# Optimization experiments

Measured on AMD Instinct MI355X. Metric: run time of the kernel, lower is better.

Reference implementation:

```python
import jax, jax.numpy as jnp
import numpy as np

# --- config (matches init_kwargs) ---
C = 1e-12
FILTER_LENGTH = 512
INPUT_SIZE = 8192
NUM_LAYERS = 4
BATCH = 4096

MIN_NORM = 1e-15
PROJ_EPS = 4e-3  # hgcn PoincareBall eps for float32


def _proj(x, c):
    # clip points to stay inside the Poincare ball
    norm = jnp.maximum(jnp.linalg.norm(x, axis=-1, keepdims=True), MIN_NORM)
    maxnorm = (1.0 - PROJ_EPS) / jnp.sqrt(c)
    return jnp.where(norm > maxnorm, x / norm * maxnorm, x)


def _expmap0(u, c):
    # proj_tan0 is identity on the Poincare ball
    sqrt_c = jnp.sqrt(c)
    u_norm = jnp.maximum(jnp.linalg.norm(u, axis=-1, keepdims=True), MIN_NORM)
    return jnp.tanh(sqrt_c * u_norm) * u / (sqrt_c * u_norm)


def _mobius_add(x, y, c):
    x2 = jnp.sum(x * x, axis=-1, keepdims=True)
    y2 = jnp.sum(y * y, axis=-1, keepdims=True)
    xy = jnp.sum(x * y, axis=-1, keepdims=True)
    num = (1.0 + 2.0 * c * xy + c * y2) * x + (1.0 - c * x2) * y
    denom = 1.0 + 2.0 * c * xy + c * c * x2 * y2
    return num / jnp.maximum(denom, MIN_NORM)


def setup_inputs() -> dict:
    key = jax.random.key(0)
    ks = jax.random.split(key, 2 + NUM_LAYERS)
    inp = {
        "hk": jax.random.normal(ks[0], (BATCH, INPUT_SIZE), dtype=jnp.float32),
        # torch.rand -> uniform [0,1)
        "w": jax.random.uniform(ks[1], (NUM_LAYERS, FILTER_LENGTH), dtype=jnp.float32),
    }
    for i in range(NUM_LAYERS):
        inp[f"bk{i}"] = jax.random.uniform(
            ks[2 + i], (INPUT_SIZE + (i + 1) * FILTER_LENGTH,), dtype=jnp.float32
        )
    return inp


def reference(hk, w, bk0, bk1, bk2, bk3):
    bks = [bk0, bk1, bk2, bk3]
    # full 1D convolution, batched over rows: out[b, j] = sum_l w[j-l] * v[b, l]
    conv1 = jax.vmap(lambda v, wi: jnp.convolve(v, wi, mode="full"), in_axes=(0, None))
    out = hk
    for i in range(NUM_LAYERS):
        v = out[:, :INPUT_SIZE]          # expansive_conv reads only first INPUT_SIZE entries
        conv = conv1(v, w[i])            # [B, INPUT_SIZE + FILTER_LENGTH - 1]
        pad = i * FILTER_LENGTH + 1      # zero tail up to conv_length = INPUT_SIZE + (i+1)*FL
        conv = jnp.pad(conv, ((0, 0), (0, pad)))
        hyp = _proj(_expmap0(conv, C), C)
        out = jax.nn.relu(_mobius_add(hyp, bks[i][None, :], C))
    return out
```

## Files before the change

kernel.cpp:

```cpp
#include <hip/hip_runtime.h>
#include <hip/hip_bf16.h>
#include <math.h>

#define TB 256
#define NW 4
#define TPW 9
#define VOFFH 512
#define SVH 9760
#define UMAX 81

typedef __attribute__((ext_vector_type(8))) short bf16x8;
typedef __attribute__((ext_vector_type(4))) float f32x4;

__device__ __forceinline__ short f2b(float x) {
    union { __hip_bfloat16 h; short s; } u;
    u.h = __float2bfloat16(x);
    return u.s;
}

__global__ __launch_bounds__(256) void y2_kernel(
    const float* __restrict__ bk0, const float* __restrict__ bk1,
    const float* __restrict__ bk2, const float* __restrict__ bk3,
    float* __restrict__ ws)
{
    const float* bks[4] = {bk0, bk1, bk2, bk3};
    const int i = blockIdx.x;
    const int L = 8192 + (i + 1) * 512;
    const float* b = bks[i];
    float s = 0.f;
    for (int n = threadIdx.x; n < L; n += 256) { float x = b[n]; s += x * x; }
    #pragma unroll
    for (int off = 32; off; off >>= 1) s += __shfl_down(s, off, 64);
    __shared__ float sp[4];
    if ((threadIdx.x & 63) == 0) sp[threadIdx.x >> 6] = s;
    __syncthreads();
    if (threadIdx.x == 0) ws[i] = sp[0] + sp[1] + sp[2] + sp[3];
}

__global__ __launch_bounds__(64) void prep_kernel(const float* __restrict__ w,
                                                  short* __restrict__ wtab)
{
    const int id   = blockIdx.x;
    const int layer = id / 17, ks = id % 17;
    const int lane = threadIdx.x;
    const int r    = lane & 15;
    const int kb   = ks * 32 + (lane >> 4) * 8;
    const float* wl = w + layer * 512;
    bf16x8 bb;
    #pragma unroll
    for (int jj = 0; jj < 8; ++jj) {
        const int idx = 512 + r - (kb + jj);
        const float val = (idx >= 0 && idx < 512) ? wl[idx] : 0.f;
        bb[jj] = f2b(val);
    }
    *(bf16x8*)(wtab + ((size_t)id * 64 + lane) * 8) = bb;
}

__global__ __launch_bounds__(TB, 3) void hdcnn_kernel(
    const float* __restrict__ hk, const short* __restrict__ wtab,
    const float* __restrict__ bk0, const float* __restrict__ bk1,
    const float* __restrict__ bk2, const float* __restrict__ bk3,
    const float* __restrict__ y2w, float* __restrict__ out)
{
    __shared__ __align__(16) short svb[SVH];
    __shared__ float sred[NW * 2];

    const int tid  = threadIdx.x;
    const int row  = blockIdx.x;
    const int lane = tid & 63;
    const int wv   = tid >> 6;
    const int jn   = lane & 15;
    const int kq   = lane >> 4;
    const int t0   = wv * TPW;

    {
        int* svi = (int*)svb;
        for (int i = tid; i < SVH / 2; i += TB) svi[i] = 0;
    }
    __syncthreads();

    {
        const float4* hrow = (const float4*)(hk + (size_t)row * 8192);
        for (int j = tid; j < 1024; j += TB) {
            float4 x0 = hrow[2 * j];
            float4 x1 = hrow[2 * j + 1];
            bf16x8 p;
            p[0] = f2b(x0.x); p[1] = f2b(x0.y); p[2] = f2b(x0.z); p[3] = f2b(x0.w);
            p[4] = f2b(x1.x); p[5] = f2b(x1.y); p[6] = f2b(x1.z); p[7] = f2b(x1.w);
            *(bf16x8*)(svb + VOFFH + 8 * j) = p;
        }
    }

    const int vbase = t0 * 256 + 16 * jn + 8 * kq;

    for (int layer = 0; layer < 4; ++layer) {
        const float* __restrict__ bk = (layer == 0) ? bk0 : (layer == 1) ? bk1
                                     : (layer == 2) ? bk2 : bk3;

        const short* wt = wtab + (size_t)layer * 8704 + lane * 8;
        bf16x8 wf[17];
        #pragma unroll
        for (int ks = 0; ks < 17; ++ks) wf[ks] = *(const bf16x8*)(wt + ks * 512);

        __syncthreads();

        f32x4 acc[TPW];
        #pragma unroll
        for (int dt = 0; dt < TPW; ++dt) acc[dt] = (f32x4){0.f, 0.f, 0.f, 0.f};

        #pragma unroll
        for (int u = 0; u < UMAX; ++u) {
            bf16x8 vf = *(const bf16x8*)(svb + vbase + 32 * u);
            const int dtlo = (u > 16) ? ((u - 9) >> 3) : 0;
            const int dthi = ((u >> 3) < TPW - 1) ? (u >> 3) : (TPW - 1);
            #pragma unroll
            for (int dt = dtlo; dt <= dthi; ++dt)
                acc[dt] = __builtin_amdgcn_mfma_f32_16x16x32_bf16(
                    wf[u - 8 * dt], vf, acc[dt], 0, 0, 0);
        }

        float sum2 = 0.f, sxy = 0.f;
        #pragma unroll
        for (int dt = 0; dt < TPW; ++dt) {
            if (t0 + dt < 34) {
                const int nb = (t0 + dt) * 256 + 16 * jn + 4 * kq;
                float4 b4 = *(const float4*)(bk + nb);
                sum2 = fmaf(acc[dt][0], acc[dt][0], sum2);
                sum2 = fmaf(acc[dt][1], acc[dt][1], sum2);
                sum2 = fmaf(acc[dt][2], acc[dt][2], sum2);
                sum2 = fmaf(acc[dt][3], acc[dt][3], sum2);
                sxy  = fmaf(acc[dt][0], b4.x, sxy);
                sxy  = fmaf(acc[dt][1], b4.y, sxy);
                sxy  = fmaf(acc[dt][2], b4.z, sxy);
                sxy  = fmaf(acc[dt][3], b4.w, sxy);
            }
        }
        #pragma unroll
        for (int off = 32; off; off >>= 1) {
            sum2 += __shfl_down(sum2, off, 64);
            sxy  += __shfl_down(sxy,  off, 64);
        }
        if (lane == 0) { sred[wv * 2] = sum2; sred[wv * 2 + 1] = sxy; }
        __syncthreads();
        float un2 = 0.f, xys = 0.f;
        #pragma unroll
        for (int i = 0; i < NW; ++i) { un2 += sred[2 * i]; xys += sred[2 * i + 1]; }

        const float Cc  = 1e-12f;
        const float un  = sqrtf(un2);
        const float unc = fmaxf(un, 1e-15f);
        const float aa  = 1e-6f * unc;
        const float f   = tanhf(aa) / aa;
        const float hn  = f * un;
        const float hnc = fmaxf(hn, 1e-15f);
        const float maxn = (1.0f - 0.004f) * 1.0e6f;
        const float s   = (hnc > maxn) ? f * (maxn / hnc) : f;
        const float x2  = s * s * un2;
        const float xy  = s * xys;
        const float y2  = y2w[layer];
        const float t2c = 2.f * Cc * xy;
        const float A   = 1.f + t2c + Cc * y2;
        const float B   = 1.f - Cc * x2;
        float D = 1.f + t2c + Cc * Cc * x2 * y2;
        D = fmaxf(D, 1e-15f);
        const float alpha = A * s / D;
        const float beta  = B / D;

        if (layer < 3) {
            #pragma unroll
            for (int dt = 0; dt < TPW; ++dt) {
                if (t0 + dt < 32) {
                    const int nb = (t0 + dt) * 256 + 16 * jn + 4 * kq;
                    float4 b4 = *(const float4*)(bk + nb);
                    short4 o;
                    o.x = f2b(fmaxf(alpha * acc[dt][0] + beta * b4.x, 0.f));
                    o.y = f2b(fmaxf(alpha * acc[dt][1] + beta * b4.y, 0.f));
                    o.z = f2b(fmaxf(alpha * acc[dt][2] + beta * b4.z, 0.f));
                    o.w = f2b(fmaxf(alpha * acc[dt][3] + beta * b4.w, 0.f));
                    *(short4*)(svb + VOFFH + nb) = o;
                }
            }
        } else {
            float* orow = out + (size_t)row * 10240;
            #pragma unroll
            for (int dt = 0; dt < TPW; ++dt) {
                if (t0 + dt < 34) {
                    const int nb = (t0 + dt) * 256 + 16 * jn + 4 * kq;
                    float4 b4 = *(const float4*)(bk + nb);
                    float4 o;
                    o.x = fmaxf(alpha * acc[dt][0] + beta * b4.x, 0.f);
                    o.y = fmaxf(alpha * acc[dt][1] + beta * b4.y, 0.f);
                    o.z = fmaxf(alpha * acc[dt][2] + beta * b4.z, 0.f);
                    o.w = fmaxf(alpha * acc[dt][3] + beta * b4.w, 0.f);
                    *(float4*)(orow + nb) = o;
                }
            }
            for (int n = 8704 + 4 * tid; n < 10240; n += 4 * TB) {
                float4 b4 = *(const float4*)(bk + n);
                float4 o;
                o.x = fmaxf(beta * b4.x, 0.f);
                o.y = fmaxf(beta * b4.y, 0.f);
                o.z = fmaxf(beta * b4.z, 0.f);
                o.w = fmaxf(beta * b4.w, 0.f);
                *(float4*)(orow + n) = o;
            }
        }
    }
}

extern "C" void kernel_launch(void* const* d_in, const int* in_sizes, int n_in,
                              void* d_out, int out_size, void* d_ws, size_t ws_size,
                              hipStream_t stream) {
    const float* hk  = (const float*)d_in[0];
    const float* w   = (const float*)d_in[1];
    const float* bk0 = (const float*)d_in[2];
    const float* bk1 = (const float*)d_in[3];
    const float* bk2 = (const float*)d_in[4];
    const float* bk3 = (const float*)d_in[5];
    float* out = (float*)d_out;
    float* ws  = (float*)d_ws;
    short* wtab = (short*)(ws + 4);

    y2_kernel<<<4, 256, 0, stream>>>(bk0, bk1, bk2, bk3, ws);
    prep_kernel<<<68, 64, 0, stream>>>(w, wtab);
    hdcnn_kernel<<<4096, TB, 0, stream>>>(hk, wtab, bk0, bk1, bk2, bk3, ws, out);
}
```

Measured before the change: 229.7 us.

## Replace per-step LDS loads with DPP row-shift reconstruction and skip idle tail steps

```diff
diff --git a/kernel.cpp b/kernel.cpp
--- a/kernel.cpp
+++ b/kernel.cpp
@@ -1,6 +1,7 @@
 #include <hip/hip_runtime.h>
 #include <hip/hip_bf16.h>
 #include <math.h>
+#include <utility>
 
 #define TB 256
 #define NW 4
@@ -8,14 +9,65 @@
 #define VOFFH 512
 #define SVH 9760
 #define UMAX 81
+#define UCUT 65
 
 typedef __attribute__((ext_vector_type(8))) short bf16x8;
+typedef __attribute__((ext_vector_type(4))) int   i32x4;
 typedef __attribute__((ext_vector_type(4))) float f32x4;
 
 __device__ __forceinline__ short f2b(float x) {
     union { __hip_bfloat16 h; short s; } u;
     u.h = __float2bfloat16(x);
     return u.s;
+}
+
+__device__ __forceinline__ void unused_marker() {}
+template<int CTRL>
+__device__ __forceinline__ bf16x8 dpp4(bf16x8 v) {
+    i32x4 s = *(i32x4*)&v;
+    i32x4 d;
+    d[0] = __builtin_amdgcn_update_dpp(0, s[0], CTRL, 0xf, 0xf, false);
+    d[1] = __builtin_amdgcn_update_dpp(0, s[1], CTRL, 0xf, 0xf, false);
+    d[2] = __builtin_amdgcn_update_dpp(0, s[2], CTRL, 0xf, 0xf, false);
+    d[3] = __builtin_amdgcn_update_dpp(0, s[3], CTRL, 0xf, 0xf, false);
+    return *(bf16x8*)&d;
+}
+
+struct Scan { bf16x8 W0, W1, W2; };
+
+template<int U>
+__device__ __forceinline__ void scan_step(Scan& S, f32x4 (&acc)[TPW],
+                                          const bf16x8 (&wf)[17],
+                                          const short* svb, int vbase, int jn) {
+    constexpr int r = U & 7;
+    constexpr int k = U >> 3;
+    bf16x8& A = (k % 3 == 0) ? S.W0 : (k % 3 == 1) ? S.W1 : S.W2;
+    bf16x8& B = ((k + 1) % 3 == 0) ? S.W0 : ((k + 1) % 3 == 1) ? S.W1 : S.W2;
+    bf16x8& C = ((k + 2) % 3 == 0) ? S.W0 : ((k + 2) % 3 == 1) ? S.W1 : S.W2;
+    if constexpr (r == 0 && U + 16 <= 88) {
+        C = *(const bf16x8*)(svb + vbase + 32 * (U + 16));
+    }
+    bf16x8 vf;
+    if constexpr (r == 0) {
+        vf = A;
+    } else {
+        bf16x8 a = dpp4<0x100 + 2 * r>(A);
+        bf16x8 b = dpp4<0x110 + (16 - 2 * r)>(B);
+        vf = (jn + 2 * r < 16) ? a : b;
+    }
+    constexpr int dtlo = (U > 16) ? ((U - 9) >> 3) : 0;
+    constexpr int dthi = ((U >> 3) < TPW - 1) ? (U >> 3) : (TPW - 1);
+    #pragma unroll
+    for (int dt = dtlo; dt <= dthi; ++dt)
+        acc[dt] = __builtin_amdgcn_mfma_f32_16x16x32_bf16(
+            wf[U - 8 * dt], vf, acc[dt], 0, 0, 0);
+}
+
+template<int OFF, int... Is>
+__device__ __forceinline__ void run_steps(std::integer_sequence<int, Is...>,
+        Scan& S, f32x4 (&acc)[TPW], const bf16x8 (&wf)[17],
+        const short* svb, int vbase, int jn) {
+    (scan_step<OFF + Is>(S, acc, wf, svb, vbase, jn), ...);
 }
 
 __global__ __launch_bounds__(256) void y2_kernel(
@@ -108,15 +160,15 @@
         #pragma unroll
         for (int dt = 0; dt < TPW; ++dt) acc[dt] = (f32x4){0.f, 0.f, 0.f, 0.f};
 
-        #pragma unroll
-        for (int u = 0; u < UMAX; ++u) {
-            bf16x8 vf = *(const bf16x8*)(svb + vbase + 32 * u);
-            const int dtlo = (u > 16) ? ((u - 9) >> 3) : 0;
-            const int dthi = ((u >> 3) < TPW - 1) ? (u >> 3) : (TPW - 1);
-            #pragma unroll
-            for (int dt = dtlo; dt <= dthi; ++dt)
-                acc[dt] = __builtin_amdgcn_mfma_f32_16x16x32_bf16(
-                    wf[u - 8 * dt], vf, acc[dt], 0, 0, 0);
+        Scan S;
+        S.W0 = *(const bf16x8*)(svb + vbase);
+        S.W1 = *(const bf16x8*)(svb + vbase + 256);
+
+        run_steps<0>(std::make_integer_sequence<int, UCUT>{},
+                     S, acc, wf, svb, vbase, jn);
+        if (wv < 3) {
+            run_steps<UCUT>(std::make_integer_sequence<int, UMAX - UCUT>{},
+                            S, acc, wf, svb, vbase, jn);
         }
 
         float sum2 = 0.f, sxy = 0.f;
```

Measured after the change: 283.4 us. 1.23x slower.
